# Optimization experiments

Hardware: AMD Instinct MI355X
Metric: run time of the kernel (lower is better)

The kernel has to match this reference:

```python
import jax, jax.numpy as jnp
import numpy as np

S, R = 512, 384            # N_seq, N_res
C_MSA, C_Z = 64, 128
C_HID, H = 32, 8
INF = 1e8
EPS = 1e-5


def _layernorm(x, w, b):
    mu = jnp.mean(x, axis=-1, keepdims=True)
    var = jnp.var(x, axis=-1, keepdims=True)
    return (x - mu) * jax.lax.rsqrt(var + EPS) * w + b


def setup_inputs() -> dict:
    key = jax.random.key(0)
    ks = jax.random.split(key, 8)
    d = {
        "m": jax.random.normal(ks[0], (S, R, C_MSA), dtype=jnp.float32),
        "z": jax.random.normal(ks[1], (R, R, C_Z), dtype=jnp.float32),
        "msa_mask": jnp.ones((S, R), dtype=jnp.float32),
        "z_mask": jnp.ones((R, R), dtype=jnp.float32),
        # learned parameters
        "ln_m_w": jnp.ones((C_MSA,), jnp.float32),
        "ln_m_b": jnp.zeros((C_MSA,), jnp.float32),
        "ln_z_w": jnp.ones((C_Z,), jnp.float32),
        "ln_z_b": jnp.zeros((C_Z,), jnp.float32),
        "w_v": jax.random.normal(ks[2], (C_MSA, H * C_HID), jnp.float32) * (1.0 / np.sqrt(C_MSA)),
        "w_g": jax.random.normal(ks[3], (C_MSA, H * C_HID), jnp.float32) * 0.02,
        "w_b": jax.random.normal(ks[4], (C_Z, H), jnp.float32) * (1.0 / np.sqrt(C_Z)),
        "w_o": jax.random.normal(ks[5], (H * C_HID, C_MSA), jnp.float32) * 0.02,
    }
    return d


def reference(m, z, msa_mask, z_mask, ln_m_w, ln_m_b, ln_z_w, ln_z_b, w_v, w_g, w_b, w_o):
    # m: [S, R, C_MSA], z: [R, R, C_Z]
    m_ln = _layernorm(m, ln_m_w, ln_m_b)
    v = (m_ln @ w_v).reshape(S, R, H, C_HID)                    # [S,R,H,C]
    g = jax.nn.sigmoid(m_ln @ w_g).reshape(S, R, H, C_HID)      # gating [S,R,H,C]
    b = _layernorm(z, ln_z_w, ln_z_b) @ w_b                     # pair bias [R,R,H]
    b = b + INF * (z_mask[..., None] - 1.0)                     # mask invalid pairs
    v = v * msa_mask[..., None, None]                           # mask MSA values
    w = jax.nn.softmax(b, axis=-2)                              # softmax over j (keys)
    # o[s,i,h,c] = sum_j w[i,j,h] * v[s,j,h,c]  (pair-weighted averaging)
    o = g * jnp.einsum('ijh,sjhd->sihd', w, v)                  # [S,R,H,C]
    out = o.reshape(S, R, H * C_HID) @ w_o                      # [S,R,C_MSA]
    return out
```

## Files before the change

### kernel.cpp

```cpp
#include <hip/hip_runtime.h>
#include <hip/hip_bf16.h>
#include <stdint.h>

#define S_DIM 512
#define R_DIM 384
#define CMSA 64
#define CZ 128
#define HH 8
#define CHID 32
#define HC 256
#define INF_V 1e8f
#define EPS_V 1e-5f

typedef __bf16 bf16x8 __attribute__((ext_vector_type(8)));
typedef float f32x4 __attribute__((ext_vector_type(4)));

__device__ __forceinline__ unsigned short f2bf(float f) {
  __hip_bfloat16 h = __float2bfloat16(f);
  return *reinterpret_cast<unsigned short*>(&h);
}
__device__ __forceinline__ float bf2f(unsigned short u) {
  __hip_bfloat16 h;
  *reinterpret_cast<unsigned short*>(&h) = u;
  return __bfloat162float(h);
}
__device__ __forceinline__ int4 pack8(const unsigned short* u) {
  int4 p;
  p.x = (int)u[0] | ((int)u[1] << 16);
  p.y = (int)u[2] | ((int)u[3] << 16);
  p.z = (int)u[4] | ((int)u[5] << 16);
  p.w = (int)u[6] | ((int)u[7] << 16);
  return p;
}

__device__ __forceinline__ float reduce8x(float* s, int cs7) {
  float t[4];
#pragma unroll
  for (int k = 0; k < 4; ++k) {
    float snd = (cs7 & 1) ? s[2 * k] : s[2 * k + 1];
    float rcv = __shfl_xor(snd, 1);
    t[k] = ((cs7 & 1) ? s[2 * k + 1] : s[2 * k]) + rcv;
  }
  float r[2];
#pragma unroll
  for (int k = 0; k < 2; ++k) {
    float snd = (cs7 & 2) ? t[2 * k] : t[2 * k + 1];
    float rcv = __shfl_xor(snd, 2);
    r[k] = ((cs7 & 2) ? t[2 * k + 1] : t[2 * k]) + rcv;
  }
  float snd = (cs7 & 4) ? r[0] : r[1];
  float rcv = __shfl_xor(snd, 4);
  return ((cs7 & 4) ? r[1] : r[0]) + rcv;
}

__global__ __launch_bounds__(256) void k_bias(
    const float* __restrict__ z, const float* __restrict__ z_mask,
    const float* __restrict__ lnw, const float* __restrict__ lnb,
    const float* __restrict__ w_b, float* __restrict__ b_out) {
  int tid = threadIdx.x, lane = tid & 63, wv = tid >> 6;
  int cs = lane & 15, ps = lane >> 4;
  int cs7 = cs & 7;

  float4 wba[2][4], wbb[2][4], lnw4[2];
  float aU[8] = {0, 0, 0, 0, 0, 0, 0, 0};
  float aA[8] = {0, 0, 0, 0, 0, 0, 0, 0};
#pragma unroll
  for (int q = 0; q < 2; ++q) {
    int c0 = q * 64 + cs * 4;
    lnw4[q] = *reinterpret_cast<const float4*>(&lnw[c0]);
    float4 lnb4 = *reinterpret_cast<const float4*>(&lnb[c0]);
#pragma unroll
    for (int e = 0; e < 4; ++e) {
      wba[q][e] = *reinterpret_cast<const float4*>(&w_b[(size_t)(c0 + e) * HH]);
      wbb[q][e] = *reinterpret_cast<const float4*>(&w_b[(size_t)(c0 + e) * HH + 4]);
      float lw = reinterpret_cast<const float*>(&lnw4[q])[e];
      float lb = reinterpret_cast<const float*>(&lnb4)[e];
      aU[0] += lw * wba[q][e].x; aU[1] += lw * wba[q][e].y;
      aU[2] += lw * wba[q][e].z; aU[3] += lw * wba[q][e].w;
      aU[4] += lw * wbb[q][e].x; aU[5] += lw * wbb[q][e].y;
      aU[6] += lw * wbb[q][e].z; aU[7] += lw * wbb[q][e].w;
      aA[0] += lb * wba[q][e].x; aA[1] += lb * wba[q][e].y;
      aA[2] += lb * wba[q][e].z; aA[3] += lb * wba[q][e].w;
      aA[4] += lb * wbb[q][e].x; aA[5] += lb * wbb[q][e].y;
      aA[6] += lb * wbb[q][e].z; aA[7] += lb * wbb[q][e].w;
    }
  }
#pragma unroll
  for (int h = 0; h < 8; ++h) {
    aU[h] += __shfl_xor(aU[h], 8);
    aA[h] += __shfl_xor(aA[h], 8);
  }
  float U_l = reduce8x(aU, cs7);
  float A_l = reduce8x(aA, cs7);

  const int NTASK = (R_DIM * R_DIM) / 4;
  for (int task = blockIdx.x * 4 + wv; task < NTASK; task += gridDim.x * 4) {
    int g = task * 4 + ps;
    const float* zp = z + (size_t)g * CZ;
    float4 zv[2];
    zv[0] = *reinterpret_cast<const float4*>(zp + cs * 4);
    zv[1] = *reinterpret_cast<const float4*>(zp + 64 + cs * 4);
    float sz = 0.f, sz2 = 0.f;
    float s[8] = {0, 0, 0, 0, 0, 0, 0, 0};
#pragma unroll
    for (int q = 0; q < 2; ++q)
#pragma unroll
      for (int e = 0; e < 4; ++e) {
        float x = reinterpret_cast<const float*>(&zv[q])[e];
        float lw = reinterpret_cast<const float*>(&lnw4[q])[e];
        sz += x; sz2 += x * x;
        float zn = x * lw;
        s[0] += zn * wba[q][e].x; s[1] += zn * wba[q][e].y;
        s[2] += zn * wba[q][e].z; s[3] += zn * wba[q][e].w;
        s[4] += zn * wbb[q][e].x; s[5] += zn * wbb[q][e].y;
        s[6] += zn * wbb[q][e].z; s[7] += zn * wbb[q][e].w;
      }
#pragma unroll
    for (int d = 1; d <= 8; d <<= 1) {
      sz += __shfl_xor(sz, d);
      sz2 += __shfl_xor(sz2, d);
    }
#pragma unroll
    for (int h = 0; h < 8; ++h) s[h] += __shfl_xor(s[h], 8);
    float S = reduce8x(s, cs7);
    float mu = sz * (1.f / CZ);
    float var = sz2 * (1.f / CZ) - mu * mu;
    float rs = rsqrtf(var + EPS_V);
    float b = rs * S + A_l - rs * mu * U_l + INF_V * (z_mask[g] - 1.f);
    if (cs < 8) {
      int i = g / R_DIM, j = g - i * R_DIM;
      b_out[((size_t)i * HH + cs) * R_DIM + j] = b;
    }
  }
}

__global__ __launch_bounds__(128) void k_softmax(
    const float* __restrict__ b_in, unsigned short* __restrict__ w_bf) {
  int row = blockIdx.x;
  int i = row / HH, h = row - i * HH;
  const float* bp = b_in + (size_t)row * R_DIM;
  int t = threadIdx.x;
  float v[3];
  float mx = -INFINITY;
#pragma unroll
  for (int k = 0; k < 3; ++k) { v[k] = bp[t + 128 * k]; mx = fmaxf(mx, v[k]); }
  __shared__ float red[128];
  red[t] = mx; __syncthreads();
  for (int off = 64; off > 0; off >>= 1) {
    if (t < off) red[t] = fmaxf(red[t], red[t + off]);
    __syncthreads();
  }
  mx = red[0]; __syncthreads();
  float sum = 0.f;
#pragma unroll
  for (int k = 0; k < 3; ++k) { v[k] = __expf(v[k] - mx); sum += v[k]; }
  red[t] = sum; __syncthreads();
  for (int off = 64; off > 0; off >>= 1) {
    if (t < off) red[t] += red[t + off];
    __syncthreads();
  }
  float inv = 1.0f / red[0];
  unsigned short* wp = w_bf + ((size_t)h * R_DIM + i) * R_DIM;
#pragma unroll
  for (int k = 0; k < 3; ++k) wp[t + 128 * k] = f2bf(v[k] * inv);
}

__global__ __launch_bounds__(256) void k_prep(
    const float* __restrict__ w_v, const float* __restrict__ w_g,
    const float* __restrict__ w_o, unsigned short* __restrict__ wv_img,
    unsigned short* __restrict__ wg_img, unsigned short* __restrict__ wo_img) {
  int gid = blockIdx.x * 256 + threadIdx.x;
  int mtx = gid >> 11, idx = gid & 2047;
  unsigned short u[8];
  if (mtx < 2) {
    const float* w = mtx ? w_g : w_v;
    unsigned short* img = mtx ? wg_img : wv_img;
    int hcr = idx >> 3, slot = idx & 7;
#pragma unroll
    for (int e = 0; e < 8; ++e) u[e] = f2bf(w[(size_t)(slot * 8 + e) * HC + hcr]);
    *reinterpret_cast<int4*>(&img[hcr * 64 + ((slot ^ (hcr & 7)) << 3)]) = pack8(u);
  } else {
    int lrow = idx >> 5, slot = idx & 31;
#pragma unroll
    for (int e = 0; e < 8; ++e) u[e] = f2bf(w_o[(size_t)(slot * 8 + e) * CMSA + lrow]);
    *reinterpret_cast<int4*>(&wo_img[lrow * 256 + ((slot ^ (lrow & 7)) << 3)]) = pack8(u);
  }
}

__global__ __launch_bounds__(512, 4) void k_vg(
    const float* __restrict__ m, const float* __restrict__ msa_mask,
    const float* __restrict__ lnw, const float* __restrict__ lnb,
    const unsigned short* __restrict__ wv_img,
    const unsigned short* __restrict__ wg_img,
    unsigned short* __restrict__ Vt, unsigned short* __restrict__ g_ws) {
  extern __shared__ char lds[];
  const int A_OFF = 0;
  const int W_OFF = 16384;
  const int M_OFF = 49152;
  int tid = threadIdx.x, l = tid & 63, wv = tid >> 6;
  int b = blockIdx.x;
  int s = b / 3;
  int res0 = (b % 3) * 128;
  size_t row0 = (size_t)s * R_DIM + res0;

  if (tid < 128) *reinterpret_cast<float*>(&lds[M_OFF + tid * 4]) = msa_mask[row0 + tid];

  {
    const int4* src = reinterpret_cast<const int4*>(wv_img);
    int4* dst = reinterpret_cast<int4*>(&lds[W_OFF]);
#pragma unroll
    for (int p = 0; p < 4; ++p) dst[p * 512 + tid] = src[p * 512 + tid];
  }

  {
    int row = tid >> 2, q = tid & 3;
    const float* mp = m + (row0 + row) * CMSA + q * 16;
    float4 x0 = *reinterpret_cast<const float4*>(mp);
    float4 x1 = *reinterpret_cast<const float4*>(mp + 4);
    float4 x2 = *reinterpret_cast<const float4*>(mp + 8);
    float4 x3 = *reinterpret_cast<const float4*>(mp + 12);
    float xs[16] = {x0.x, x0.y, x0.z, x0.w, x1.x, x1.y, x1.z, x1.w,
                    x2.x, x2.y, x2.z, x2.w, x3.x, x3.y, x3.z, x3.w};
    float sm = 0.f, s2 = 0.f;
#pragma unroll
    for (int e = 0; e < 16; ++e) { sm += xs[e]; s2 += xs[e] * xs[e]; }
    sm += __shfl_xor(sm, 1); s2 += __shfl_xor(s2, 1);
    sm += __shfl_xor(sm, 2); s2 += __shfl_xor(s2, 2);
    float mu = sm * (1.f / 64.f);
    float var = s2 * (1.f / 64.f) - mu * mu;
    float rs = rsqrtf(var + EPS_V);
    const float* lwp = lnw + q * 16;
    const float* lbp = lnb + q * 16;
    unsigned short u[16];
#pragma unroll
    for (int e = 0; e < 16; ++e)
      u[e] = f2bf((xs[e] - mu) * rs * lwp[e] + lbp[e]);
    int base = A_OFF + row * 128;
    *reinterpret_cast<int4*>(&lds[base + (((2 * q) ^ (row & 7)) << 4)]) = pack8(u);
    *reinterpret_cast<int4*>(&lds[base + (((2 * q + 1) ^ (row & 7)) << 4)]) = pack8(u + 8);
  }
  __syncthreads();

  f32x4 zz = {0.f, 0.f, 0.f, 0.f};

  {
    f32x4 vacc[2][8];
#pragma unroll
    for (int a = 0; a < 2; ++a)
#pragma unroll
      for (int n = 0; n < 8; ++n) vacc[a][n] = zz;
#pragma unroll
    for (int kc = 0; kc < 2; ++kc) {
      bf16x8 aw[2];
#pragma unroll
      for (int mfa = 0; mfa < 2; ++mfa) {
        int row = wv * 32 + mfa * 16 + (l & 15);
        aw[mfa] = *reinterpret_cast<const bf16x8*>(
            &lds[W_OFF + row * 128 + (((kc * 4 + (l >> 4)) ^ (row & 7)) << 4)]);
      }
#pragma unroll
      for (int nh = 0; nh < 2; ++nh) {
        bf16x8 bl[4];
#pragma unroll
        for (int nf = 0; nf < 4; ++nf) {
          int res = (nh * 4 + nf) * 16 + (l & 15);
          bl[nf] = *reinterpret_cast<const bf16x8*>(
              &lds[A_OFF + res * 128 + (((kc * 4 + (l >> 4)) ^ (res & 7)) << 4)]);
        }
#pragma unroll
        for (int mfa = 0; mfa < 2; ++mfa)
#pragma unroll
          for (int nf = 0; nf < 4; ++nf)
            vacc[mfa][nh * 4 + nf] =
                __builtin_amdgcn_mfma_f32_16x16x32_bf16(aw[mfa], bl[nf], vacc[mfa][nh * 4 + nf], 0, 0, 0);
      }
    }
    float mk[8];
#pragma unroll
    for (int nf = 0; nf < 8; ++nf)
      mk[nf] = *reinterpret_cast<const float*>(&lds[M_OFF + (nf * 16 + (l & 15)) * 4]);
#pragma unroll
    for (int mfa = 0; mfa < 2; ++mfa)
#pragma unroll
      for (int nf = 0; nf < 8; ++nf) {
#pragma unroll
        for (int reg = 0; reg < 4; ++reg) {
          int hc = wv * 32 + mfa * 16 + (l >> 4) * 4 + reg;
          Vt[((size_t)s * HC + hc) * R_DIM + res0 + nf * 16 + (l & 15)] =
              f2bf(vacc[mfa][nf][reg] * mk[nf]);
        }
      }
  }
  __syncthreads();

  {
    const int4* src = reinterpret_cast<const int4*>(wg_img);
    int4* dst = reinterpret_cast<int4*>(&lds[W_OFF]);
#pragma unroll
    for (int p = 0; p < 4; ++p) dst[p * 512 + tid] = src[p * 512 + tid];
  }
  __syncthreads();

  {
    int resb = (wv & 3) * 32, hcb = (wv >> 2) * 128;
    f32x4 gacc[2][8];
#pragma unroll
    for (int a = 0; a < 2; ++a)
#pragma unroll
      for (int n = 0; n < 8; ++n) gacc[a][n] = zz;
#pragma unroll
    for (int kc = 0; kc < 2; ++kc) {
      bf16x8 al[2];
#pragma unroll
      for (int mfa = 0; mfa < 2; ++mfa) {
        int row = resb + mfa * 16 + (l & 15);
        al[mfa] = *reinterpret_cast<const bf16x8*>(
            &lds[A_OFF + row * 128 + (((kc * 4 + (l >> 4)) ^ (row & 7)) << 4)]);
      }
#pragma unroll
      for (int nh = 0; nh < 2; ++nh) {
        bf16x8 bw[4];
#pragma unroll
        for (int nf = 0; nf < 4; ++nf) {
          int col = hcb + (nh * 4 + nf) * 16 + (l & 15);
          bw[nf] = *reinterpret_cast<const bf16x8*>(
              &lds[W_OFF + col * 128 + (((kc * 4 + (l >> 4)) ^ (col & 7)) << 4)]);
        }
#pragma unroll
        for (int mfa = 0; mfa < 2; ++mfa)
#pragma unroll
          for (int nf = 0; nf < 4; ++nf)
            gacc[mfa][nh * 4 + nf] =
                __builtin_amdgcn_mfma_f32_16x16x32_bf16(al[mfa], bw[nf], gacc[mfa][nh * 4 + nf], 0, 0, 0);
      }
    }
#pragma unroll
    for (int mfa = 0; mfa < 2; ++mfa)
#pragma unroll
      for (int nf = 0; nf < 8; ++nf) {
#pragma unroll
        for (int reg = 0; reg < 4; ++reg) {
          int res = resb + mfa * 16 + (l >> 4) * 4 + reg;
          int hc = hcb + nf * 16 + (l & 15);
          float sg = 1.f / (1.f + __expf(-gacc[mfa][nf][reg]));
          g_ws[(row0 + res) * HC + hc] = f2bf(sg);
        }
      }
  }
}

__global__ __launch_bounds__(512) void k_wavg(
    const unsigned short* __restrict__ Vt, const unsigned short* __restrict__ g_ws,
    const unsigned short* __restrict__ w_bf, const unsigned short* __restrict__ wo_img,
    float* __restrict__ out) {
  extern __shared__ char lds[];
  const int A_OFF = 0;
  const int B_OFF = 32768;
  const int P_OFF = 45056;
  const int W_OFF = 94208;
  int tid = threadIdx.x, l = tid & 63, wv = tid >> 6;
  int bs = blockIdx.x >> 2, bi = blockIdx.x & 3;
  int s0 = bs * 8, i0 = bi * 96;

  {
    const int4* src = reinterpret_cast<const int4*>(wo_img);
    int4* dst = reinterpret_cast<int4*>(&lds[W_OFF]);
#pragma unroll
    for (int p = 0; p < 4; ++p) dst[p * 512 + tid] = src[p * 512 + tid];
  }

  int slotg = tid & 3;
  int rA0 = tid >> 2, rA1 = 128 + (tid >> 2);
  size_t vtb0 = ((size_t)(s0 + (rA0 >> 5)) * HC + (rA0 & 31)) * R_DIM + slotg * 8;
  size_t vtb1 = ((size_t)(s0 + (rA1 >> 5)) * HC + (rA1 & 31)) * R_DIM + slotg * 8;
  int ldsA0 = rA0 * 64 + ((slotg ^ (rA0 & 3)) << 4);
  int ldsA1 = rA1 * 64 + ((slotg ^ (rA1 & 3)) << 4);
  int rB = tid >> 2;
  size_t wbase = (size_t)(i0 + rB) * R_DIM + slotg * 8;
  int ldsB = rB * 64 + ((slotg ^ (rB & 3)) << 4);

  int aoff[4], boff[3], poff[6];
#pragma unroll
  for (int mf = 0; mf < 4; ++mf) {
    int row = ((wv & 3) * 4 + mf) * 16 + (l & 15);
    aoff[mf] = row * 64 + (((l >> 4) ^ (row & 3)) << 4);
  }
#pragma unroll
  for (int nf = 0; nf < 3; ++nf) {
    int row = ((wv >> 2) * 3 + nf) * 16 + (l & 15);
    boff[nf] = row * 64 + (((l >> 4) ^ (row & 3)) << 4);
  }
#pragma unroll
  for (int mf = 0; mf < 6; ++mf) {
    int row = (wv * 6 + mf) * 16 + (l & 15);
    poff[mf] = row * 64 + (((l >> 4) ^ (row & 3)) << 4);
  }

  f32x4 zz = {0.f, 0.f, 0.f, 0.f};
  f32x4 pacc[6][4];
#pragma unroll
  for (int a = 0; a < 6; ++a)
#pragma unroll
    for (int n = 0; n < 4; ++n) pacc[a][n] = zz;

  for (int h = 0; h < 8; ++h) {
    const unsigned short* VtA = Vt + (size_t)h * 32 * R_DIM;
    const unsigned short* WB = w_bf + (size_t)h * R_DIM * R_DIM;
    f32x4 acc[4][3];
#pragma unroll
    for (int a = 0; a < 4; ++a)
#pragma unroll
      for (int n = 0; n < 3; ++n) acc[a][n] = zz;

    {
      int4 va0 = *reinterpret_cast<const int4*>(VtA + vtb0);
      int4 va1 = *reinterpret_cast<const int4*>(VtA + vtb1);
      int4 vb;
      if (tid < 384) vb = *reinterpret_cast<const int4*>(WB + wbase);
      *reinterpret_cast<int4*>(&lds[A_OFF + ldsA0]) = va0;
      *reinterpret_cast<int4*>(&lds[A_OFF + ldsA1]) = va1;
      if (tid < 384) *reinterpret_cast<int4*>(&lds[B_OFF + ldsB]) = vb;
    }
    __syncthreads();

    for (int t = 0; t < 12; ++t) {
      int cur = t & 1;
      int4 va0, va1, vb;
      if (t < 11) {
        int j0n = (t + 1) * 32;
        va0 = *reinterpret_cast<const int4*>(VtA + vtb0 + j0n);
        va1 = *reinterpret_cast<const int4*>(VtA + vtb1 + j0n);
        if (tid < 384) vb = *reinterpret_cast<const int4*>(WB + wbase + j0n);
      }
      const char* ab = &lds[A_OFF + cur * 16384];
      const char* bb = &lds[B_OFF + cur * 6144];
      bf16x8 af[4], bfr[3];
#pragma unroll
      for (int mf = 0; mf < 4; ++mf) af[mf] = *reinterpret_cast<const bf16x8*>(ab + aoff[mf]);
#pragma unroll
      for (int nf = 0; nf < 3; ++nf) bfr[nf] = *reinterpret_cast<const bf16x8*>(bb + boff[nf]);
#pragma unroll
      for (int mf = 0; mf < 4; ++mf)
#pragma unroll
        for (int nf = 0; nf < 3; ++nf)
          acc[mf][nf] = __builtin_amdgcn_mfma_f32_16x16x32_bf16(af[mf], bfr[nf], acc[mf][nf], 0, 0, 0);
      if (t < 11) {
        int nxt = cur ^ 1;
        *reinterpret_cast<int4*>(&lds[A_OFF + nxt * 16384 + ldsA0]) = va0;
        *reinterpret_cast<int4*>(&lds[A_OFF + nxt * 16384 + ldsA1]) = va1;
        if (tid < 384) *reinterpret_cast<int4*>(&lds[B_OFF + nxt * 6144 + ldsB]) = vb;
      }
      __syncthreads();
    }

#pragma unroll
    for (int mf = 0; mf < 4; ++mf) {
      int MT = (wv & 3) * 4 + mf;
      int sl = MT >> 1;
      int c0 = (MT & 1) * 16 + (l >> 4) * 4;
#pragma unroll
      for (int nf = 0; nf < 3; ++nf) {
        int il = ((wv >> 2) * 3 + nf) * 16 + (l & 15);
        size_t gidx = ((size_t)(s0 + sl) * R_DIM + i0 + il) * HC + h * 32 + c0;
        ushort4 g4 = *reinterpret_cast<const ushort4*>(g_ws + gidx);
        int prow = sl * 96 + il;
        ushort4 og;
        og.x = f2bf(acc[mf][nf][0] * bf2f(g4.x));
        og.y = f2bf(acc[mf][nf][1] * bf2f(g4.y));
        og.z = f2bf(acc[mf][nf][2] * bf2f(g4.z));
        og.w = f2bf(acc[mf][nf][3] * bf2f(g4.w));
        *reinterpret_cast<ushort4*>(
            &lds[P_OFF + prow * 64 + (((c0 >> 3) ^ (prow & 3)) << 4) + (c0 & 7) * 2]) = og;
      }
    }
    __syncthreads();

    {
      bf16x8 pa[6], bw[4];
#pragma unroll
      for (int nt = 0; nt < 4; ++nt) {
        int lrow = nt * 16 + (l & 15);
        bw[nt] = *reinterpret_cast<const bf16x8*>(
            &lds[W_OFF + lrow * 512 + (((h * 4 + (l >> 4)) ^ (lrow & 7)) << 4)]);
      }
#pragma unroll
      for (int mf = 0; mf < 6; ++mf) pa[mf] = *reinterpret_cast<const bf16x8*>(&lds[P_OFF + poff[mf]]);
#pragma unroll
      for (int mf = 0; mf < 6; ++mf)
#pragma unroll
        for (int nt = 0; nt < 4; ++nt)
          pacc[mf][nt] = __builtin_amdgcn_mfma_f32_16x16x32_bf16(pa[mf], bw[nt], pacc[mf][nt], 0, 0, 0);
    }
    __syncthreads();
  }

#pragma unroll
  for (int mf = 0; mf < 6; ++mf) {
#pragma unroll
    for (int reg = 0; reg < 4; ++reg) {
      int prow = (wv * 6 + mf) * 16 + (l >> 4) * 4 + reg;
      int sl = prow / 96;
      int il = prow - sl * 96;
      size_t orow = (size_t)(s0 + sl) * R_DIM + i0 + il;
#pragma unroll
      for (int nt = 0; nt < 4; ++nt)
        out[orow * CMSA + nt * 16 + (l & 15)] = pacc[mf][nt][reg];
    }
  }
}

extern "C" void kernel_launch(void* const* d_in, const int* in_sizes, int n_in,
                              void* d_out, int out_size, void* d_ws, size_t ws_size,
                              hipStream_t stream) {
  (void)in_sizes; (void)n_in; (void)out_size; (void)ws_size;
  const float* m        = (const float*)d_in[0];
  const float* z        = (const float*)d_in[1];
  const float* msa_mask = (const float*)d_in[2];
  const float* z_mask   = (const float*)d_in[3];
  const float* ln_m_w   = (const float*)d_in[4];
  const float* ln_m_b   = (const float*)d_in[5];
  const float* ln_z_w   = (const float*)d_in[6];
  const float* ln_z_b   = (const float*)d_in[7];
  const float* w_v      = (const float*)d_in[8];
  const float* w_g      = (const float*)d_in[9];
  const float* w_b      = (const float*)d_in[10];
  const float* w_o      = (const float*)d_in[11];
  float* out = (float*)d_out;

  char* ws = (char*)d_ws;
  unsigned short* Vt   = (unsigned short*)ws;
  unsigned short* g_ws = (unsigned short*)(ws + 100663296ull);
  float*          b_ws = (float*)(ws + 201326592ull);
  unsigned short* w_bf = (unsigned short*)(ws + 206045184ull);
  unsigned short* wv_img = (unsigned short*)(ws + 201326592ull);
  unsigned short* wg_img = (unsigned short*)(ws + 201326592ull + 32768ull);
  unsigned short* wo_img = (unsigned short*)(ws + 201326592ull + 65536ull);

  k_bias<<<dim3(2304), dim3(256), 0, stream>>>(
      z, z_mask, ln_z_w, ln_z_b, w_b, b_ws);
  k_softmax<<<dim3(R_DIM * HH), dim3(128), 0, stream>>>(b_ws, w_bf);
  k_prep<<<dim3(24), dim3(256), 0, stream>>>(
      w_v, w_g, w_o, wv_img, wg_img, wo_img);
  k_vg<<<dim3(S_DIM * R_DIM / 128), dim3(512), 49664, stream>>>(
      m, msa_mask, ln_m_w, ln_m_b, wv_img, wg_img, Vt, g_ws);
  k_wavg<<<dim3(256), dim3(512), 126976, stream>>>(Vt, g_ws, w_bf, wo_img, out);
}
```

Measured before the change: 347.0 us.

## Halve k_wavg tile, drop LDS W_o staging, swizzle block order

Halves the per-block sequence tile of the weighted-average kernel from 8 to 4 sequences, doubling the grid to 512 blocks. LDS use drops from about 124KB to 52KB by reading W_o fragments straight from global memory instead of staging them in shared memory. Launch bounds now request higher occupancy. A block-index permutation changes which blocks run together, meant to improve cache sharing of the w_bf and Vt tiles. The intent is more resident blocks per CU and better latency hiding, at the cost of more total global reads of w_bf, since each block now covers fewer sequences per weight tile.

```diff
diff --git a/kernel.cpp b/kernel.cpp
--- a/kernel.cpp
+++ b/kernel.cpp
@@ -349,40 +349,32 @@
   }
 }
 
-__global__ __launch_bounds__(512) void k_wavg(
+__global__ __launch_bounds__(512, 4) void k_wavg(
     const unsigned short* __restrict__ Vt, const unsigned short* __restrict__ g_ws,
     const unsigned short* __restrict__ w_bf, const unsigned short* __restrict__ wo_img,
     float* __restrict__ out) {
   extern __shared__ char lds[];
   const int A_OFF = 0;
-  const int B_OFF = 32768;
-  const int P_OFF = 45056;
-  const int W_OFF = 94208;
+  const int B_OFF = 16384;
+  const int P_OFF = 28672;
   int tid = threadIdx.x, l = tid & 63, wv = tid >> 6;
-  int bs = blockIdx.x >> 2, bi = blockIdx.x & 3;
-  int s0 = bs * 8, i0 = bi * 96;
-
-  {
-    const int4* src = reinterpret_cast<const int4*>(wo_img);
-    int4* dst = reinterpret_cast<int4*>(&lds[W_OFF]);
-#pragma unroll
-    for (int p = 0; p < 4; ++p) dst[p * 512 + tid] = src[p * 512 + tid];
-  }
+  int p = blockIdx.x;
+  int L = ((p & 7) << 6) | (p >> 3);
+  int bs = L >> 2, bi = L & 3;
+  int s0 = bs * 4, i0 = bi * 96;
 
   int slotg = tid & 3;
-  int rA0 = tid >> 2, rA1 = 128 + (tid >> 2);
-  size_t vtb0 = ((size_t)(s0 + (rA0 >> 5)) * HC + (rA0 & 31)) * R_DIM + slotg * 8;
-  size_t vtb1 = ((size_t)(s0 + (rA1 >> 5)) * HC + (rA1 & 31)) * R_DIM + slotg * 8;
-  int ldsA0 = rA0 * 64 + ((slotg ^ (rA0 & 3)) << 4);
-  int ldsA1 = rA1 * 64 + ((slotg ^ (rA1 & 3)) << 4);
+  int rA = tid >> 2;
+  size_t vtb = ((size_t)(s0 + (rA >> 5)) * HC + (rA & 31)) * R_DIM + slotg * 8;
+  int ldsA = rA * 64 + ((slotg ^ (rA & 3)) << 4);
   int rB = tid >> 2;
   size_t wbase = (size_t)(i0 + rB) * R_DIM + slotg * 8;
   int ldsB = rB * 64 + ((slotg ^ (rB & 3)) << 4);
 
-  int aoff[4], boff[3], poff[6];
-#pragma unroll
-  for (int mf = 0; mf < 4; ++mf) {
-    int row = ((wv & 3) * 4 + mf) * 16 + (l & 15);
+  int aoff[2], boff[3], poff[3];
+#pragma unroll
+  for (int mf = 0; mf < 2; ++mf) {
+    int row = ((wv & 3) * 2 + mf) * 16 + (l & 15);
     aoff[mf] = row * 64 + (((l >> 4) ^ (row & 3)) << 4);
   }
 #pragma unroll
@@ -391,71 +383,75 @@
     boff[nf] = row * 64 + (((l >> 4) ^ (row & 3)) << 4);
   }
 #pragma unroll
-  for (int mf = 0; mf < 6; ++mf) {
-    int row = (wv * 6 + mf) * 16 + (l & 15);
+  for (int mf = 0; mf < 3; ++mf) {
+    int row = (wv * 3 + mf) * 16 + (l & 15);
     poff[mf] = row * 64 + (((l >> 4) ^ (row & 3)) << 4);
   }
 
   f32x4 zz = {0.f, 0.f, 0.f, 0.f};
-  f32x4 pacc[6][4];
-#pragma unroll
-  for (int a = 0; a < 6; ++a)
+  f32x4 pacc[3][4];
+#pragma unroll
+  for (int a = 0; a < 3; ++a)
 #pragma unroll
     for (int n = 0; n < 4; ++n) pacc[a][n] = zz;
 
   for (int h = 0; h < 8; ++h) {
     const unsigned short* VtA = Vt + (size_t)h * 32 * R_DIM;
     const unsigned short* WB = w_bf + (size_t)h * R_DIM * R_DIM;
-    f32x4 acc[4][3];
-#pragma unroll
-    for (int a = 0; a < 4; ++a)
+    f32x4 acc[2][3];
+#pragma unroll
+    for (int a = 0; a < 2; ++a)
 #pragma unroll
       for (int n = 0; n < 3; ++n) acc[a][n] = zz;
 
     {
-      int4 va0 = *reinterpret_cast<const int4*>(VtA + vtb0);
-      int4 va1 = *reinterpret_cast<const int4*>(VtA + vtb1);
+      int4 va = *reinterpret_cast<const int4*>(VtA + vtb);
       int4 vb;
       if (tid < 384) vb = *reinterpret_cast<const int4*>(WB + wbase);
-      *reinterpret_cast<int4*>(&lds[A_OFF + ldsA0]) = va0;
-      *reinterpret_cast<int4*>(&lds[A_OFF + ldsA1]) = va1;
+      *reinterpret_cast<int4*>(&lds[A_OFF + ldsA]) = va;
       if (tid < 384) *reinterpret_cast<int4*>(&lds[B_OFF + ldsB]) = vb;
     }
     __syncthreads();
 
     for (int t = 0; t < 12; ++t) {
       int cur = t & 1;
-      int4 va0, va1, vb;
+      int4 va, vb;
       if (t < 11) {
         int j0n = (t + 1) * 32;
-        va0 = *reinterpret_cast<const int4*>(VtA + vtb0 + j0n);
-        va1 = *reinterpret_cast<const int4*>(VtA + vtb1 + j0n);
+        va = *reinterpret_cast<const int4*>(VtA + vtb + j0n);
         if (tid < 384) vb = *reinterpret_cast<const int4*>(WB + wbase + j0n);
       }
-      const char* ab = &lds[A_OFF + cur * 16384];
+      const char* ab = &lds[A_OFF + cur * 8192];
       const char* bb = &lds[B_OFF + cur * 6144];
-      bf16x8 af[4], bfr[3];
-#pragma unroll
-      for (int mf = 0; mf < 4; ++mf) af[mf] = *reinterpret_cast<const bf16x8*>(ab + aoff[mf]);
+      bf16x8 af[2], bfr[3];
+#pragma unroll
+      for (int mf = 0; mf < 2; ++mf) af[mf] = *reinterpret_cast<const bf16x8*>(ab + aoff[mf]);
 #pragma unroll
       for (int nf = 0; nf < 3; ++nf) bfr[nf] = *reinterpret_cast<const bf16x8*>(bb + boff[nf]);
 #pragma unroll
-      for (int mf = 0; mf < 4; ++mf)
+      for (int mf = 0; mf < 2; ++mf)
 #pragma unroll
         for (int nf = 0; nf < 3; ++nf)
           acc[mf][nf] = __builtin_amdgcn_mfma_f32_16x16x32_bf16(af[mf], bfr[nf], acc[mf][nf], 0, 0, 0);
       if (t < 11) {
         int nxt = cur ^ 1;
-        *reinterpret_cast<int4*>(&lds[A_OFF + nxt * 16384 + ldsA0]) = va0;
-        *reinterpret_cast<int4*>(&lds[A_OFF + nxt * 16384 + ldsA1]) = va1;
+        *reinterpret_cast<int4*>(&lds[A_OFF + nxt * 8192 + ldsA]) = va;
         if (tid < 384) *reinterpret_cast<int4*>(&lds[B_OFF + nxt * 6144 + ldsB]) = vb;
       }
       __syncthreads();
     }
 
-#pragma unroll
-    for (int mf = 0; mf < 4; ++mf) {
-      int MT = (wv & 3) * 4 + mf;
+    bf16x8 bw[4];
+#pragma unroll
+    for (int nt = 0; nt < 4; ++nt) {
+      int lrow = nt * 16 + (l & 15);
+      bw[nt] = *reinterpret_cast<const bf16x8*>(
+          &wo_img[lrow * 256 + (((h * 4 + (l >> 4)) ^ (lrow & 7)) << 3)]);
+    }
+
+#pragma unroll
+    for (int mf = 0; mf < 2; ++mf) {
+      int MT = (wv & 3) * 2 + mf;
       int sl = MT >> 1;
       int c0 = (MT & 1) * 16 + (l >> 4) * 4;
 #pragma unroll
@@ -476,17 +472,11 @@
     __syncthreads();
 
     {
-      bf16x8 pa[6], bw[4];
-#pragma unroll
-      for (int nt = 0; nt < 4; ++nt) {
-        int lrow = nt * 16 + (l & 15);
-        bw[nt] = *reinterpret_cast<const bf16x8*>(
-            &lds[W_OFF + lrow * 512 + (((h * 4 + (l >> 4)) ^ (lrow & 7)) << 4)]);
-      }
-#pragma unroll
-      for (int mf = 0; mf < 6; ++mf) pa[mf] = *reinterpret_cast<const bf16x8*>(&lds[P_OFF + poff[mf]]);
-#pragma unroll
-      for (int mf = 0; mf < 6; ++mf)
+      bf16x8 pa[3];
+#pragma unroll
+      for (int mf = 0; mf < 3; ++mf) pa[mf] = *reinterpret_cast<const bf16x8*>(&lds[P_OFF + poff[mf]]);
+#pragma unroll
+      for (int mf = 0; mf < 3; ++mf)
 #pragma unroll
         for (int nt = 0; nt < 4; ++nt)
           pacc[mf][nt] = __builtin_amdgcn_mfma_f32_16x16x32_bf16(pa[mf], bw[nt], pacc[mf][nt], 0, 0, 0);
@@ -495,10 +485,10 @@
   }
 
 #pragma unroll
-  for (int mf = 0; mf < 6; ++mf) {
+  for (int mf = 0; mf < 3; ++mf) {
 #pragma unroll
     for (int reg = 0; reg < 4; ++reg) {
-      int prow = (wv * 6 + mf) * 16 + (l >> 4) * 4 + reg;
+      int prow = (wv * 3 + mf) * 16 + (l >> 4) * 4 + reg;
       int sl = prow / 96;
       int il = prow - sl * 96;
       size_t orow = (size_t)(s0 + sl) * R_DIM + i0 + il;
@@ -543,5 +533,5 @@
       w_v, w_g, w_o, wv_img, wg_img, wo_img);
   k_vg<<<dim3(S_DIM * R_DIM / 128), dim3(512), 49664, stream>>>(
       m, msa_mask, ln_m_w, ln_m_b, wv_img, wg_img, Vt, g_ws);
-  k_wavg<<<dim3(256), dim3(512), 126976, stream>>>(Vt, g_ws, w_bf, wo_img, out);
-}
+  k_wavg<<<dim3(512), dim3(512), 53248, stream>>>(Vt, g_ws, w_bf, wo_img, out);
+}
```

New measurement: 379.4 us. 1.09x slower.
